# Optimization experiments

Measured on AMD Instinct MI355X. Metric: run time of the kernel, lower is better.

## Reference

```python
import jax, jax.numpy as jnp
import numpy as np

EMBED_DIM = 1024
NUM_HEADS = 16
HEAD_DIM = EMBED_DIM // NUM_HEADS
B, S = 2, 2048


def setup_inputs() -> dict:
    key = jax.random.key(0)
    k = jax.random.split(key, 8)
    scale = 1.0 / np.sqrt(EMBED_DIM)
    return {
        "x": jax.random.normal(k[0], (B, S, EMBED_DIM), dtype=jnp.float32),
        "x1": jax.random.normal(k[1], (B, S, EMBED_DIM), dtype=jnp.float32),
        "x2": jax.random.normal(k[2], (B, S, EMBED_DIM), dtype=jnp.float32),
        "qkv_w": jax.random.normal(k[3], (3 * EMBED_DIM, EMBED_DIM), dtype=jnp.float32) * scale,
        "qkv_b": jnp.zeros((3 * EMBED_DIM,), dtype=jnp.float32),
        "out_w": jax.random.normal(k[4], (EMBED_DIM, EMBED_DIM), dtype=jnp.float32) * scale,
        "out_b": jnp.zeros((EMBED_DIM,), dtype=jnp.float32),
    }


def reference(x, x1, x2, qkv_w, qkv_b, out_w, out_b):
    # x1, x2 are accepted but unused, matching the torch module.
    b, s, e = x.shape
    qkv = x @ qkv_w.T + qkv_b                      # [B,S,3E]
    qkv = qkv.reshape(b, s, 3, NUM_HEADS, HEAD_DIM)
    qkv = jnp.transpose(qkv, (2, 0, 3, 1, 4))      # [3,B,H,S,D]
    q, k, v = qkv[0], qkv[1], qkv[2]
    scores = jnp.einsum("bhqd,bhkd->bhqk", q, k) / np.sqrt(HEAD_DIM)
    probs = jax.nn.sigmoid(scores)                 # [B,H,S,S]
    sample = jax.random.bernoulli(jax.random.key(42), probs).astype(probs.dtype)
    # straight-through: forward uses sample, gradient flows as identity to probs
    attn = probs + jax.lax.stop_gradient(sample - probs)
    out = jnp.einsum("bhqk,bhkd->bhqd", attn, v)   # [B,H,S,D]
    out = jnp.transpose(out, (0, 2, 1, 3)).reshape(b, s, e)
    return out @ out_w.T + out_b
```

## Files before the change

kernel.cpp:

```cpp
#include <hip/hip_runtime.h>
#include <stdint.h>

#define NB 2
#define NS 2048
#define NE 1024
#define NH 16
#define ND 64

typedef __attribute__((ext_vector_type(8))) short short8;
typedef __attribute__((ext_vector_type(4))) float f4;
typedef __attribute__((ext_vector_type(4))) unsigned short us4;

static __device__ __forceinline__ unsigned short bf16_rne(float x) {
  uint32_t u = __builtin_bit_cast(uint32_t, x);
  u += 0x7fffu + ((u >> 16) & 1u);
  return (unsigned short)(u >> 16);
}
static __device__ __forceinline__ float bf16_f32(unsigned short h) {
  uint32_t u = ((uint32_t)h) << 16;
  return __builtin_bit_cast(float, u);
}

static __device__ __forceinline__ void threefry42(uint32_t x0, uint32_t x1,
                                                  uint32_t& o0, uint32_t& o1) {
  const uint32_t ks0 = 0u, ks1 = 42u;
  const uint32_t ks2 = 0u ^ 42u ^ 0x1BD11BDAu;
  x0 += ks0; x1 += ks1;
#define TF4(a,b,c,d) \
  x0 += x1; x1 = __builtin_rotateleft32(x1, a); x1 ^= x0; \
  x0 += x1; x1 = __builtin_rotateleft32(x1, b); x1 ^= x0; \
  x0 += x1; x1 = __builtin_rotateleft32(x1, c); x1 ^= x0; \
  x0 += x1; x1 = __builtin_rotateleft32(x1, d); x1 ^= x0;
  TF4(13,15,26,6)  x0 += ks1; x1 += ks2 + 1u;
  TF4(17,29,16,24) x0 += ks2; x1 += ks0 + 2u;
  TF4(13,15,26,6)  x0 += ks0; x1 += ks1 + 3u;
  TF4(17,29,16,24) x0 += ks1; x1 += ks2 + 4u;
  TF4(13,15,26,6)  x0 += ks2; x1 += ks0 + 5u;
#undef TF4
  o0 = x0; o1 = x1;
}

static __device__ __forceinline__ void gl2lds16(const void* g, void* l) {
  __builtin_amdgcn_global_load_lds(
      (const __attribute__((address_space(1))) uint32_t*)g,
      (__attribute__((address_space(3))) uint32_t*)l, 16, 0, 0);
}

__global__ void k_split(const float* __restrict__ x, const float* __restrict__ qw,
                        const float* __restrict__ ow,
                        unsigned short* __restrict__ xh, unsigned short* __restrict__ xl,
                        unsigned short* __restrict__ wh, unsigned short* __restrict__ wl,
                        unsigned short* __restrict__ woh) {
  for (uint32_t i = blockIdx.x * 256u + threadIdx.x; i < 8388608u; i += gridDim.x * 256u) {
    if (i < 4194304u) {
      float v = x[i];
      unsigned short hi = bf16_rne(v);
      xh[i] = hi;
      xl[i] = bf16_rne(v - bf16_f32(hi));
    } else if (i < 7340032u) {
      uint32_t j = i - 4194304u;
      float v = qw[j];
      unsigned short hi = bf16_rne(v);
      wh[j] = hi;
      wl[j] = bf16_rne(v - bf16_f32(hi));
    } else {
      uint32_t j = i - 7340032u;
      woh[j] = bf16_rne(ow[j]);
    }
  }
}

__global__ __launch_bounds__(256) void k_qkv(
    const unsigned short* __restrict__ xh, const unsigned short* __restrict__ xl,
    const unsigned short* __restrict__ wh, const unsigned short* __restrict__ wl,
    const float* __restrict__ qkv_b,
    unsigned short* __restrict__ Qh, unsigned short* __restrict__ Ql,
    unsigned short* __restrict__ Kh, unsigned short* __restrict__ Kl,
    unsigned short* __restrict__ Vt) {
  __shared__ unsigned short SM[16384];
  unsigned short* Ah = SM;
  unsigned short* Al = SM + 4096;
  unsigned short* Bh = SM + 8192;
  unsigned short* Bl = SM + 12288;
  const int tid = threadIdx.x;
  const int lane = tid & 63, wid = tid >> 6;
  const int wm = wid >> 1, wn = wid & 1;
  const int bn = blockIdx.x, bm = blockIdx.y;
  const bool isV = (bn >= 16);
  const int quad = lane >> 4, c16 = lane & 15;
  const int ldrow = lane >> 2;
  const int ldk = (lane & 3) * 8;

  f4 acc[4][4];
#pragma unroll
  for (int a = 0; a < 4; ++a)
#pragma unroll
    for (int b = 0; b < 4; ++b) { f4 z = {0.f, 0.f, 0.f, 0.f}; acc[a][b] = z; }

  for (int kt = 0; kt < 32; ++kt) {
    const int k0 = kt * 32;
    __syncthreads();
#pragma unroll
    for (int r = 0; r < 2; ++r) {
      const int c = wid + r * 4;
      const int grow = c * 16 + ldrow;
      const size_t ao = (size_t)(bm * 128 + grow) * 1024 + k0 + ldk;
      const size_t bo = (size_t)(bn * 128 + grow) * 1024 + k0 + ldk;
      const int lo = c * 512 + lane * 8;
      gl2lds16(xh + ao, &Ah[lo]);
      gl2lds16(wh + bo, &Bh[lo]);
      if (!isV) {
        gl2lds16(xl + ao, &Al[lo]);
        gl2lds16(wl + bo, &Bl[lo]);
      }
    }
    __syncthreads();

    short8 ah[4], al[4], bhf[4], blf[4];
#pragma unroll
    for (int t = 0; t < 4; ++t) {
      ah[t] = *(const short8*)&Ah[(wm * 64 + t * 16 + c16) * 32 + quad * 8];
      bhf[t] = *(const short8*)&Bh[(wn * 64 + t * 16 + c16) * 32 + quad * 8];
      if (!isV) {
        al[t] = *(const short8*)&Al[(wm * 64 + t * 16 + c16) * 32 + quad * 8];
        blf[t] = *(const short8*)&Bl[(wn * 64 + t * 16 + c16) * 32 + quad * 8];
      }
    }
    if (isV) {
#pragma unroll
      for (int tm = 0; tm < 4; ++tm)
#pragma unroll
        for (int tn = 0; tn < 4; ++tn)
          acc[tm][tn] = __builtin_amdgcn_mfma_f32_16x16x32_bf16(ah[tm], bhf[tn], acc[tm][tn], 0, 0, 0);
    } else {
#pragma unroll
      for (int tm = 0; tm < 4; ++tm)
#pragma unroll
        for (int tn = 0; tn < 4; ++tn) {
          acc[tm][tn] = __builtin_amdgcn_mfma_f32_16x16x32_bf16(ah[tm], bhf[tn], acc[tm][tn], 0, 0, 0);
          acc[tm][tn] = __builtin_amdgcn_mfma_f32_16x16x32_bf16(ah[tm], blf[tn], acc[tm][tn], 0, 0, 0);
          acc[tm][tn] = __builtin_amdgcn_mfma_f32_16x16x32_bf16(al[tm], bhf[tn], acc[tm][tn], 0, 0, 0);
        }
    }
  }

  if (!isV) {
#pragma unroll
    for (int tm = 0; tm < 4; ++tm) {
#pragma unroll
      for (int tn = 0; tn < 4; ++tn) {
        const int j = bn * 128 + wn * 64 + tn * 16 + c16;
        const float bias = qkv_b[j];
        const int which = j >> 10;
        const int rem = j & 1023;
        const int h = rem >> 6, d = rem & 63;
#pragma unroll
        for (int r = 0; r < 4; ++r) {
          const int i = bm * 128 + wm * 64 + tm * 16 + quad * 4 + r;
          const int b = i >> 11, s = i & 2047;
          const size_t off = (((size_t)(b * 16 + h)) * 2048 + (size_t)s) * 64 + d;
          const float v = acc[tm][tn][r] + bias;
          const unsigned short hi = bf16_rne(v);
          const unsigned short lo = bf16_rne(v - bf16_f32(hi));
          if (which == 0) { Qh[off] = hi; Ql[off] = lo; }
          else            { Kh[off] = hi; Kl[off] = lo; }
        }
      }
    }
  } else {
    __syncthreads();
#pragma unroll
    for (int tm = 0; tm < 4; ++tm) {
#pragma unroll
      for (int tn = 0; tn < 4; ++tn) {
        const int j = bn * 128 + wn * 64 + tn * 16 + c16;
        const float bias = qkv_b[j];
        const int d_local = wn * 64 + tn * 16 + c16;
#pragma unroll
        for (int r = 0; r < 4; ++r) {
          const int s_local = wm * 64 + tm * 16 + quad * 4 + r;
          SM[d_local * 128 + s_local] = bf16_rne(acc[tm][tn][r] + bias);
        }
      }
    }
    __syncthreads();
    const int b = (bm * 128) >> 11;
    const int s0 = (bm * 128) & 2047;
    const int h2 = (bn - 16) * 2;
#pragma unroll
    for (int it = 0; it < 8; ++it) {
      const int chunk = it * 256 + tid;
      const int dr = chunk >> 4;
      const int sc = (chunk & 15) * 8;
      const short8 v = *(const short8*)&SM[dr * 128 + sc];
      const int bh = b * 16 + h2 + (dr >> 6);
      const int d = dr & 63;
      *(short8*)&Vt[((size_t)bh * 64 + d) * 2048 + s0 + sc] = v;
    }
  }
}

__global__ __launch_bounds__(256) void k_attn(
    const unsigned short* __restrict__ Qh, const unsigned short* __restrict__ Ql,
    const unsigned short* __restrict__ Khg, const unsigned short* __restrict__ Klg,
    const unsigned short* __restrict__ Vtg, unsigned short* __restrict__ AO) {
  __shared__ unsigned short Ksh[4096], Ksl[4096], Vs[8192];
  const int tid = threadIdx.x;
  const int lane = tid & 63, w = tid >> 6;
  const int quad = lane >> 4, c16 = lane & 15;
  const int q0 = blockIdx.x * 64;
  const int bh = blockIdx.y;
  const int ks = blockIdx.z;
  const int kbase = ks * 1024;
  const size_t base = (size_t)bh * (size_t)(2048 * 64);
  unsigned short* AOp = AO + (size_t)ks * 4194304u;

  const size_t qoff = base + (size_t)(q0 + w * 16 + c16) * 64 + quad * 8;
  const short8 qh0 = *(const short8*)&Qh[qoff];
  const short8 qh1 = *(const short8*)&Qh[qoff + 32];
  const short8 ql0 = *(const short8*)&Ql[qoff];
  const short8 ql1 = *(const short8*)&Ql[qoff + 32];

  const uint32_t fb = (uint32_t)bh * 4194304u +
                      (uint32_t)(q0 + w * 16 + quad * 4) * 2048u + (uint32_t)c16;

  const int c0 = tid, r0 = c0 >> 3, g0 = ((c0 & 7) - r0) & 7;
  const int c1 = tid + 256, r1 = c1 >> 3, g1 = ((c1 & 7) - r1) & 7;

  const int lsb = (((c16 >> 2) << 4) + ((quad & 1) << 3)) << 2;
  const int bitsel = ((quad >> 1) << 2) + (c16 & 3);

  f4 oacc[4];
#pragma unroll
  for (int s = 0; s < 4; ++s) { f4 z = {0.f, 0.f, 0.f, 0.f}; oacc[s] = z; }

  auto stage = [&](int kb, int vbuf) {
    const size_t koff = base + (size_t)kb * 64;
    gl2lds16(Khg + koff + r0 * 64 + g0 * 8, &Ksh[c0 * 8]);
    gl2lds16(Klg + koff + r0 * 64 + g0 * 8, &Ksl[c0 * 8]);
    gl2lds16(Vtg + base + (size_t)r0 * 2048 + kb + g0 * 8, &Vs[vbuf * 4096 + c0 * 8]);
    gl2lds16(Khg + koff + r1 * 64 + g1 * 8, &Ksh[c1 * 8]);
    gl2lds16(Klg + koff + r1 * 64 + g1 * 8, &Ksl[c1 * 8]);
    gl2lds16(Vtg + base + (size_t)r1 * 2048 + kb + g1 * 8, &Vs[vbuf * 4096 + c1 * 8]);
  };

  stage(kbase, 0);

  for (int kt = 0; kt < 16; ++kt) {
    const int kb = kbase + kt * 64;
    const int vb = (kt & 1) * 4096;
    __syncthreads();

    f4 sacc[4];
#pragma unroll
    for (int sub = 0; sub < 4; ++sub) {
      const int rK = sub * 16 + c16;
      const int sA = ((quad + rK) & 7) * 8;
      const int sB = ((quad + 4 + rK) & 7) * 8;
      const short8 kh0 = *(const short8*)&Ksh[rK * 64 + sA];
      const short8 kh1 = *(const short8*)&Ksh[rK * 64 + sB];
      const short8 kl0 = *(const short8*)&Ksl[rK * 64 + sA];
      const short8 kl1 = *(const short8*)&Ksl[rK * 64 + sB];
      f4 s = {0.f, 0.f, 0.f, 0.f};
      s = __builtin_amdgcn_mfma_f32_16x16x32_bf16(qh0, kh0, s, 0, 0, 0);
      s = __builtin_amdgcn_mfma_f32_16x16x32_bf16(qh1, kh1, s, 0, 0, 0);
      s = __builtin_amdgcn_mfma_f32_16x16x32_bf16(qh0, kl0, s, 0, 0, 0);
      s = __builtin_amdgcn_mfma_f32_16x16x32_bf16(qh1, kl1, s, 0, 0, 0);
      s = __builtin_amdgcn_mfma_f32_16x16x32_bf16(ql0, kh0, s, 0, 0, 0);
      s = __builtin_amdgcn_mfma_f32_16x16x32_bf16(ql1, kh1, s, 0, 0, 0);
      sacc[sub] = s;
    }
    __syncthreads();
    if (kt < 15) stage(kb + 64, (kt & 1) ^ 1);

    uint32_t pk = 0u;
#pragma unroll
    for (int sub = 0; sub < 4; ++sub) {
#pragma unroll
      for (int rr = 0; rr < 4; ++rr) {
        const uint32_t f = fb + (uint32_t)(rr * 2048) + (uint32_t)(kb + sub * 16);
        uint32_t o0, o1;
        threefry42(0u, f, o0, o1);
        const float m = (float)((o0 ^ o1) >> 9);
        const float e = __builtin_amdgcn_exp2f(sacc[sub][rr] * -0.18033688f);
        if (fmaf(m, e, m) < 8388608.0f) pk |= (1u << (sub * 4 + rr));
      }
    }

    short8 pa0, pa1;
#pragma unroll
    for (int j = 0; j < 8; ++j) {
      const uint32_t t =
          ((uint32_t)__builtin_amdgcn_ds_bpermute(lsb + j * 4, (int)pk)) >> bitsel;
      pa0[j] = (t & 1u) ? (short)0x3F80 : (short)0;
      pa1[j] = (t & 256u) ? (short)0x3F80 : (short)0;
    }
#pragma unroll
    for (int sub = 0; sub < 4; ++sub) {
      const int rV = sub * 16 + c16;
      const short8 vv0 = *(const short8*)&Vs[vb + rV * 64 + ((quad + rV) & 7) * 8];
      const short8 vv1 = *(const short8*)&Vs[vb + rV * 64 + ((quad + 4 + rV) & 7) * 8];
      oacc[sub] = __builtin_amdgcn_mfma_f32_16x16x32_bf16(pa0, vv0, oacc[sub], 0, 0, 0);
      oacc[sub] = __builtin_amdgcn_mfma_f32_16x16x32_bf16(pa1, vv1, oacc[sub], 0, 0, 0);
    }
  }

  const int b = bh >> 4, hh = bh & 15;
#pragma unroll
  for (int sub = 0; sub < 4; ++sub)
#pragma unroll
    for (int r = 0; r < 4; ++r) {
      const int srow = b * 2048 + q0 + w * 16 + quad * 4 + r;
      AOp[(size_t)srow * 1024 + hh * 64 + sub * 16 + c16] = bf16_rne(oacc[sub][r]);
    }
}

__global__ __launch_bounds__(256) void k_out(
    const unsigned short* __restrict__ A0, const unsigned short* __restrict__ A1,
    const unsigned short* __restrict__ Bw,
    const float* __restrict__ out_b, float* __restrict__ out) {
  __shared__ unsigned short As[128 * 32], Bs[128 * 32];
  const int tid = threadIdx.x;
  const int lane = tid & 63, wid = tid >> 6;
  const int wm = wid >> 1, wn = wid & 1;
  const int bn = blockIdx.x, bm = blockIdx.y;
  const int quad = lane >> 4, c16 = lane & 15;
  const int ldrow = lane >> 2;
  const int ldk = (lane & 3) * 8;

  f4 acc[4][4];
#pragma unroll
  for (int a = 0; a < 4; ++a)
#pragma unroll
    for (int b = 0; b < 4; ++b) { f4 z = {0.f, 0.f, 0.f, 0.f}; acc[a][b] = z; }

  for (int kt = 0; kt < 32; ++kt) {
    const int k0 = kt * 32;
    __syncthreads();
#pragma unroll
    for (int r = 0; r < 2; ++r) {
      const int c = wid + r * 4;
      const int grow = c * 16 + ldrow;
      const size_t ao = (size_t)(bm * 128 + grow) * 1024 + k0 + ldk;
      const size_t bo = (size_t)(bn * 128 + grow) * 1024 + k0 + ldk;
      const int lo = c * 512 + lane * 8;
      const short8 a0 = *(const short8*)&A0[ao];
      const short8 a1 = *(const short8*)&A1[ao];
      short8 acm;
#pragma unroll
      for (int j = 0; j < 8; ++j)
        acm[j] = (short)bf16_rne(bf16_f32((unsigned short)a0[j]) +
                                 bf16_f32((unsigned short)a1[j]));
      *(short8*)&As[lo] = acm;
      gl2lds16(Bw + bo, &Bs[lo]);
    }
    __syncthreads();

    short8 af[4], bf[4];
#pragma unroll
    for (int t = 0; t < 4; ++t) {
      af[t] = *(const short8*)&As[(wm * 64 + t * 16 + c16) * 32 + quad * 8];
      bf[t] = *(const short8*)&Bs[(wn * 64 + t * 16 + c16) * 32 + quad * 8];
    }
#pragma unroll
    for (int tm = 0; tm < 4; ++tm)
#pragma unroll
      for (int tn = 0; tn < 4; ++tn)
        acc[tm][tn] = __builtin_amdgcn_mfma_f32_16x16x32_bf16(af[tm], bf[tn], acc[tm][tn], 0, 0, 0);
  }

#pragma unroll
  for (int tm = 0; tm < 4; ++tm) {
#pragma unroll
    for (int tn = 0; tn < 4; ++tn) {
      const int j = bn * 128 + wn * 64 + tn * 16 + c16;
      const float bias = out_b[j];
#pragma unroll
      for (int r = 0; r < 4; ++r) {
        const int i = bm * 128 + wm * 64 + tm * 16 + quad * 4 + r;
        out[(size_t)i * 1024 + j] = acc[tm][tn][r] + bias;
      }
    }
  }
}

extern "C" void kernel_launch(void* const* d_in, const int* in_sizes, int n_in,
                              void* d_out, int out_size, void* d_ws, size_t ws_size,
                              hipStream_t stream) {
  const float* x     = (const float*)d_in[0];
  const float* qkv_w = (const float*)d_in[3];
  const float* qkv_b = (const float*)d_in[4];
  const float* out_w = (const float*)d_in[5];
  const float* out_b = (const float*)d_in[6];
  float* out = (float*)d_out;

  unsigned short* xh  = (unsigned short*)d_ws;
  unsigned short* xl  = xh + 4194304;
  unsigned short* wh  = xl + 4194304;
  unsigned short* wl  = wh + 3145728;
  unsigned short* woh = wl + 3145728;
  unsigned short* Vt  = woh + 1048576;
  unsigned short* Qh  = Vt + 4194304;
  unsigned short* Ql  = Qh + 4194304;
  unsigned short* Kh  = Ql + 4194304;
  unsigned short* Kl  = Kh + 4194304;
  unsigned short* AO0 = xh;
  unsigned short* AO1 = xl;

  k_split<<<8192, 256, 0, stream>>>(x, qkv_w, out_w, xh, xl, wh, wl, woh);
  k_qkv<<<dim3(24, 32), 256, 0, stream>>>(xh, xl, wh, wl, qkv_b, Qh, Ql, Kh, Kl, Vt);
  k_attn<<<dim3(32, 32, 2), 256, 0, stream>>>(Qh, Ql, Kh, Kl, Vt, AO0);
  k_out<<<dim3(8, 32), 256, 0, stream>>>(AO0, AO1, woh, out_b, out);
}
```

Before: 539.6 us.

## Switch attention kernel to 32x32 MFMA tiles with 128-query blocks

Rewrites the attention kernel to use 32x32x16 bf16 MFMAs in transposed form (K as A operand, Q as B), so each wave handles 32 query rows and the block covers 128 queries instead of 64. This halves the number of blocks and the K/V LDS staging per query. It also simplifies the probability-bit redistribution to a single swap bpermute. Each wave now does twice the RNG work per tile and holds more registers (larger accumulators and Q fragments), which may reduce occupancy.

```diff
diff --git a/kernel.cpp b/kernel.cpp
--- a/kernel.cpp
+++ b/kernel.cpp
@@ -9,6 +9,7 @@
 
 typedef __attribute__((ext_vector_type(8))) short short8;
 typedef __attribute__((ext_vector_type(4))) float f4;
+typedef __attribute__((ext_vector_type(16))) float f16v;
 typedef __attribute__((ext_vector_type(4))) unsigned short us4;
 
 static __device__ __forceinline__ unsigned short bf16_rne(float x) {
@@ -207,32 +208,28 @@
   __shared__ unsigned short Ksh[4096], Ksl[4096], Vs[8192];
   const int tid = threadIdx.x;
   const int lane = tid & 63, w = tid >> 6;
-  const int quad = lane >> 4, c16 = lane & 15;
-  const int q0 = blockIdx.x * 64;
+  const int l31 = lane & 31, h = lane >> 5;
+  const int q0 = blockIdx.x * 128;
   const int bh = blockIdx.y;
   const int ks = blockIdx.z;
   const int kbase = ks * 1024;
   const size_t base = (size_t)bh * (size_t)(2048 * 64);
   unsigned short* AOp = AO + (size_t)ks * 4194304u;
-
-  const size_t qoff = base + (size_t)(q0 + w * 16 + c16) * 64 + quad * 8;
-  const short8 qh0 = *(const short8*)&Qh[qoff];
-  const short8 qh1 = *(const short8*)&Qh[qoff + 32];
-  const short8 ql0 = *(const short8*)&Ql[qoff];
-  const short8 ql1 = *(const short8*)&Ql[qoff + 32];
-
-  const uint32_t fb = (uint32_t)bh * 4194304u +
-                      (uint32_t)(q0 + w * 16 + quad * 4) * 2048u + (uint32_t)c16;
+  const int q_lane = q0 + w * 32 + l31;
+
+  const size_t qoff = base + (size_t)q_lane * 64 + h * 8;
+  short8 qhf[4], qlf[4];
+#pragma unroll
+  for (int ds = 0; ds < 4; ++ds) {
+    qhf[ds] = *(const short8*)&Qh[qoff + ds * 16];
+    qlf[ds] = *(const short8*)&Ql[qoff + ds * 16];
+  }
+
+  const uint32_t Fq = (uint32_t)bh * 4194304u + (uint32_t)q_lane * 2048u + 4u * (uint32_t)h;
 
   const int c0 = tid, r0 = c0 >> 3, g0 = ((c0 & 7) - r0) & 7;
   const int c1 = tid + 256, r1 = c1 >> 3, g1 = ((c1 & 7) - r1) & 7;
-
-  const int lsb = (((c16 >> 2) << 4) + ((quad & 1) << 3)) << 2;
-  const int bitsel = ((quad >> 1) << 2) + (c16 & 3);
-
-  f4 oacc[4];
-#pragma unroll
-  for (int s = 0; s < 4; ++s) { f4 z = {0.f, 0.f, 0.f, 0.f}; oacc[s] = z; }
+  const int swidx = (lane ^ 32) << 2;
 
   auto stage = [&](int kb, int vbuf) {
     const size_t koff = base + (size_t)kb * 64;
@@ -244,75 +241,102 @@
     gl2lds16(Vtg + base + (size_t)r1 * 2048 + kb + g1 * 8, &Vs[vbuf * 4096 + c1 * 8]);
   };
 
+  f16v oacc0 = {0.f,0.f,0.f,0.f,0.f,0.f,0.f,0.f,0.f,0.f,0.f,0.f,0.f,0.f,0.f,0.f};
+  f16v oacc1 = oacc0;
+
   stage(kbase, 0);
+
+  auto sample16 = [&](const f16v& s, uint32_t F) -> uint32_t {
+    uint32_t pk = 0u;
+#pragma unroll
+    for (int rg = 0; rg < 16; ++rg) {
+      uint32_t o0, o1;
+      threefry42(0u, F + (uint32_t)((rg & 3) + 8 * (rg >> 2)), o0, o1);
+      const float m = (float)((o0 ^ o1) >> 9);
+      const float e = __builtin_amdgcn_exp2f(s[rg] * -0.18033688f);
+      if (fmaf(m, e, m) < 8388608.0f) pk |= (1u << rg);
+    }
+    return pk;
+  };
+
+  auto pv16 = [&](uint32_t pk, int km, int vb) {
+    const uint32_t pksw = (uint32_t)__builtin_amdgcn_ds_bpermute(swidx, (int)pk);
+    const uint32_t ph0 = h ? pksw : pk;
+    const uint32_t ph1 = h ? pk : pksw;
+#pragma unroll
+    for (int k2 = 0; k2 < 2; ++k2) {
+      const int bb = (k2 * 2 + h) * 4;
+      const uint32_t nl = (ph0 >> bb) & 15u;
+      const uint32_t nh = (ph1 >> bb) & 15u;
+      short8 pf;
+#pragma unroll
+      for (int j = 0; j < 4; ++j) {
+        pf[j]     = (nl & (1u << j)) ? (short)0x3F80 : (short)0;
+        pf[j + 4] = (nh & (1u << j)) ? (short)0x3F80 : (short)0;
+      }
+      const int vch = (km * 2 + k2) * 2 + h;
+#pragma unroll
+      for (int dm = 0; dm < 2; ++dm) {
+        const int vrow = dm * 32 + l31;
+        const short8 vf = *(const short8*)&Vs[vb + vrow * 64 + ((vch + vrow) & 7) * 8];
+        if (dm == 0) oacc0 = __builtin_amdgcn_mfma_f32_32x32x16_bf16(vf, pf, oacc0, 0, 0, 0);
+        else         oacc1 = __builtin_amdgcn_mfma_f32_32x32x16_bf16(vf, pf, oacc1, 0, 0, 0);
+      }
+    }
+  };
 
   for (int kt = 0; kt < 16; ++kt) {
     const int kb = kbase + kt * 64;
     const int vb = (kt & 1) * 4096;
     __syncthreads();
 
-    f4 sacc[4];
-#pragma unroll
-    for (int sub = 0; sub < 4; ++sub) {
-      const int rK = sub * 16 + c16;
-      const int sA = ((quad + rK) & 7) * 8;
-      const int sB = ((quad + 4 + rK) & 7) * 8;
-      const short8 kh0 = *(const short8*)&Ksh[rK * 64 + sA];
-      const short8 kh1 = *(const short8*)&Ksh[rK * 64 + sB];
-      const short8 kl0 = *(const short8*)&Ksl[rK * 64 + sA];
-      const short8 kl1 = *(const short8*)&Ksl[rK * 64 + sB];
-      f4 s = {0.f, 0.f, 0.f, 0.f};
-      s = __builtin_amdgcn_mfma_f32_16x16x32_bf16(qh0, kh0, s, 0, 0, 0);
-      s = __builtin_amdgcn_mfma_f32_16x16x32_bf16(qh1, kh1, s, 0, 0, 0);
-      s = __builtin_amdgcn_mfma_f32_16x16x32_bf16(qh0, kl0, s, 0, 0, 0);
-      s = __builtin_amdgcn_mfma_f32_16x16x32_bf16(qh1, kl1, s, 0, 0, 0);
-      s = __builtin_amdgcn_mfma_f32_16x16x32_bf16(ql0, kh0, s, 0, 0, 0);
-      s = __builtin_amdgcn_mfma_f32_16x16x32_bf16(ql1, kh1, s, 0, 0, 0);
-      sacc[sub] = s;
-    }
+    f16v s0 = {0.f,0.f,0.f,0.f,0.f,0.f,0.f,0.f,0.f,0.f,0.f,0.f,0.f,0.f,0.f,0.f};
+    f16v s1 = s0;
+    {
+      const int krow0 = l31, krow1 = 32 + l31;
+#pragma unroll
+      for (int ds = 0; ds < 4; ++ds) {
+        const int ch = ds * 2 + h;
+        const int off0 = krow0 * 64 + ((ch + krow0) & 7) * 8;
+        const int off1 = krow1 * 64 + ((ch + krow1) & 7) * 8;
+        const short8 kh0 = *(const short8*)&Ksh[off0];
+        const short8 kl0 = *(const short8*)&Ksl[off0];
+        const short8 kh1 = *(const short8*)&Ksh[off1];
+        const short8 kl1 = *(const short8*)&Ksl[off1];
+        s0 = __builtin_amdgcn_mfma_f32_32x32x16_bf16(kh0, qhf[ds], s0, 0, 0, 0);
+        s0 = __builtin_amdgcn_mfma_f32_32x32x16_bf16(kh0, qlf[ds], s0, 0, 0, 0);
+        s0 = __builtin_amdgcn_mfma_f32_32x32x16_bf16(kl0, qhf[ds], s0, 0, 0, 0);
+        s1 = __builtin_amdgcn_mfma_f32_32x32x16_bf16(kh1, qhf[ds], s1, 0, 0, 0);
+        s1 = __builtin_amdgcn_mfma_f32_32x32x16_bf16(kh1, qlf[ds], s1, 0, 0, 0);
+        s1 = __builtin_amdgcn_mfma_f32_32x32x16_bf16(kl1, qhf[ds], s1, 0, 0, 0);
+      }
+    }
+
+    const uint32_t F0 = Fq + (uint32_t)kb;
+    const uint32_t pk0 = sample16(s0, F0);
+
     __syncthreads();
     if (kt < 15) stage(kb + 64, (kt & 1) ^ 1);
 
-    uint32_t pk = 0u;
-#pragma unroll
-    for (int sub = 0; sub < 4; ++sub) {
-#pragma unroll
-      for (int rr = 0; rr < 4; ++rr) {
-        const uint32_t f = fb + (uint32_t)(rr * 2048) + (uint32_t)(kb + sub * 16);
-        uint32_t o0, o1;
-        threefry42(0u, f, o0, o1);
-        const float m = (float)((o0 ^ o1) >> 9);
-        const float e = __builtin_amdgcn_exp2f(sacc[sub][rr] * -0.18033688f);
-        if (fmaf(m, e, m) < 8388608.0f) pk |= (1u << (sub * 4 + rr));
-      }
-    }
-
-    short8 pa0, pa1;
-#pragma unroll
-    for (int j = 0; j < 8; ++j) {
-      const uint32_t t =
-          ((uint32_t)__builtin_amdgcn_ds_bpermute(lsb + j * 4, (int)pk)) >> bitsel;
-      pa0[j] = (t & 1u) ? (short)0x3F80 : (short)0;
-      pa1[j] = (t & 256u) ? (short)0x3F80 : (short)0;
-    }
-#pragma unroll
-    for (int sub = 0; sub < 4; ++sub) {
-      const int rV = sub * 16 + c16;
-      const short8 vv0 = *(const short8*)&Vs[vb + rV * 64 + ((quad + rV) & 7) * 8];
-      const short8 vv1 = *(const short8*)&Vs[vb + rV * 64 + ((quad + 4 + rV) & 7) * 8];
-      oacc[sub] = __builtin_amdgcn_mfma_f32_16x16x32_bf16(pa0, vv0, oacc[sub], 0, 0, 0);
-      oacc[sub] = __builtin_amdgcn_mfma_f32_16x16x32_bf16(pa1, vv1, oacc[sub], 0, 0, 0);
-    }
+    pv16(pk0, 0, vb);
+    const uint32_t pk1 = sample16(s1, F0 + 32u);
+    pv16(pk1, 1, vb);
   }
 
   const int b = bh >> 4, hh = bh & 15;
-#pragma unroll
-  for (int sub = 0; sub < 4; ++sub)
-#pragma unroll
-    for (int r = 0; r < 4; ++r) {
-      const int srow = b * 2048 + q0 + w * 16 + quad * 4 + r;
-      AOp[(size_t)srow * 1024 + hh * 64 + sub * 16 + c16] = bf16_rne(oacc[sub][r]);
-    }
+  const size_t rowbase = ((size_t)(b * 2048 + q_lane)) * 1024 + hh * 64;
+#pragma unroll
+  for (int dm = 0; dm < 2; ++dm) {
+#pragma unroll
+    for (int a = 0; a < 4; ++a) {
+      us4 v;
+#pragma unroll
+      for (int c = 0; c < 4; ++c)
+        v[c] = bf16_rne(dm == 0 ? oacc0[a * 4 + c] : oacc1[a * 4 + c]);
+      const int d0 = dm * 32 + 8 * a + 4 * h;
+      *(us4*)&AOp[rowbase + d0] = v;
+    }
+  }
 }
 
 __global__ __launch_bounds__(256) void k_out(
@@ -409,6 +433,6 @@
 
   k_split<<<8192, 256, 0, stream>>>(x, qkv_w, out_w, xh, xl, wh, wl, woh);
   k_qkv<<<dim3(24, 32), 256, 0, stream>>>(xh, xl, wh, wl, qkv_b, Qh, Ql, Kh, Kl, Vt);
-  k_attn<<<dim3(32, 32, 2), 256, 0, stream>>>(Qh, Ql, Kh, Kl, Vt, AO0);
+  k_attn<<<dim3(16, 32, 2), 256, 0, stream>>>(Qh, Ql, Kh, Kl, Vt, AO0);
   k_out<<<dim3(8, 32), 256, 0, stream>>>(AO0, AO1, woh, out_b, out);
 }
```

Measured after the change: 536.3 us. About the same (-0.6%).
